# Optimization experiments

Hardware: AMD Instinct MI355X
Metric: run time of the kernel (lower is better)

The kernel has to match this reference:

```python
import jax, jax.numpy as jnp
import numpy as np

TAG = 64
START = 0
END = 1
NEG = -10000.0


def setup_inputs() -> dict:
    key = jax.random.key(0)
    kf, kw, kl = jax.random.split(key, 3)
    B, T, K = 1024, 512, TAG
    feats = jax.random.normal(kf, (B, T, K), dtype=jnp.float32)
    w = jax.random.uniform(kw, (K, K), minval=-1.0 / K, maxval=1.0 / K, dtype=jnp.float32)
    # default adjacency: forbid transitions into start (row START) and out of end (col END)
    adj = jnp.zeros((K, K), jnp.float32).at[START, :].set(1.0).at[:, END].set(1.0)
    weights = w + NEG * adj
    lens = jax.random.randint(kl, (B,), 1, T + 1)  # 1..T inclusive
    return {"feats": feats, "weights": weights, "lens": lens}


def reference(feats, weights, lens):
    # feats: [B, T, K], weights: [K, K] with weights[next, prev], lens: [B]
    B, T, K = feats.shape
    init = jnp.full((B, K), NEG, feats.dtype).at[:, START].set(0.0)
    mask_tb = (jnp.arange(T)[None, :] < lens[:, None]).T  # [T, B]
    ident = jnp.arange(K, dtype=jnp.int32)

    def step(fv, inp):
        feat, m = inp  # feat: [B, K], m: [B]
        scores = fv[:, None, :] + weights[None, :, :]  # [B, next, prev]
        new_fv = jnp.max(scores, axis=-1) + feat       # emission added after max
        bptr = jnp.argmax(scores, axis=-1).astype(jnp.int32)
        fv2 = jnp.where(m[:, None], new_fv, fv)
        bptr2 = jnp.where(m[:, None], bptr, ident[None, :])  # identity keeps backtrace valid past len
        return fv2, bptr2

    fv, bptrs = jax.lax.scan(step, init, (jnp.swapaxes(feats, 0, 1), mask_tb))
    terminal = fv + weights[END][None, :]              # transition to end tag
    best_last = jnp.argmax(terminal, axis=-1)
    path_score = jnp.take_along_axis(terminal, best_last[:, None], axis=1)[:, 0]

    def back(tag, bp):  # tag: [B], bp: [B, K]
        prev = jnp.take_along_axis(bp, tag[:, None], axis=1)[:, 0]
        return prev, tag  # emit tag chosen at this timestep

    _, path = jax.lax.scan(back, best_last.astype(jnp.int32), bptrs, reverse=True)
    best_paths = jnp.swapaxes(path, 0, 1)  # [B, T]; positions >= lens[b] are padding
    return path_score, best_paths
```

## Files before the change

### kernel.cpp

```cpp
#include <hip/hip_runtime.h>

#define TAGS 64
#define MAXT 512
#define NEG  -10000.0f
#define CH   8

__global__ __launch_bounds__(64, 1) void crf_viterbi(
    const float* __restrict__ feats,
    const float* __restrict__ weights,
    const int*   __restrict__ lens,
    float*       __restrict__ out,
    int B, int T)
{
    const int b    = blockIdx.x;
    const int lane = threadIdx.x;
    const int len  = lens[b];

    __shared__ float fv[TAGS];
    __shared__ float fbuf[2][CH * TAGS];
    __shared__ unsigned char  bptr[MAXT * TAGS];
    __shared__ unsigned short path[MAXT];

    float4 w4[16];
    #pragma unroll
    for (int i = 0; i < 16; ++i)
        w4[i] = *reinterpret_cast<const float4*>(weights + lane * TAGS + i * 4);
    const float wEnd = weights[1 * TAGS + lane];

    fv[lane] = (lane == 0) ? 0.0f : NEG;

    const float* fb  = feats + (size_t)b * T * TAGS;
    const int    lim = len * TAGS - 4;

    float nf = NEG;

#define F3(a, b, c) fmaxf(fmaxf((a), (b)), (c))
#define M3(a, b, c) min(min((a), (b)), (c))

    auto step = [&](int cbuf, int i, int t) {
        const float feat = fbuf[cbuf][i * TAGS + lane];
        float4 fq[16];
        #pragma unroll
        for (int g = 0; g < 16; ++g)
            fq[g] = *reinterpret_cast<const float4*>(&fv[g * 4]);
        float4 c4[16];
        #pragma unroll
        for (int g = 0; g < 16; ++g) {
            c4[g].x = fq[g].x + w4[g].x;
            c4[g].y = fq[g].y + w4[g].y;
            c4[g].z = fq[g].z + w4[g].z;
            c4[g].w = fq[g].w + w4[g].w;
        }
        const float* c = reinterpret_cast<const float*>(c4);

        float v1[22];
        #pragma unroll
        for (int k = 0; k < 21; ++k) v1[k] = F3(c[3*k], c[3*k+1], c[3*k+2]);
        v1[21] = c[63];
        float v2[8];
        #pragma unroll
        for (int k = 0; k < 7; ++k) v2[k] = F3(v1[3*k], v1[3*k+1], v1[3*k+2]);
        v2[7] = v1[21];
        const float v30 = F3(v2[0], v2[1], v2[2]);
        const float v31 = F3(v2[3], v2[4], v2[5]);
        const float v32 = fmaxf(v2[6], v2[7]);
        const float m   = F3(v30, v31, v32);

        nf = m + feat;
        fv[lane] = nf;

        unsigned e[64];
        #pragma unroll
        for (int p = 0; p < 64; ++p) {
            const float d = m - c[p];
            e[p] = (__float_as_uint(d) & 0xFFFFFFC0u) | (unsigned)p;
        }
        unsigned u1[22];
        #pragma unroll
        for (int k = 0; k < 21; ++k) u1[k] = M3(e[3*k], e[3*k+1], e[3*k+2]);
        u1[21] = e[63];
        unsigned u2[8];
        #pragma unroll
        for (int k = 0; k < 7; ++k) u2[k] = M3(u1[3*k], u1[3*k+1], u1[3*k+2]);
        u2[7] = u1[21];
        const unsigned u30 = M3(u2[0], u2[1], u2[2]);
        const unsigned u31 = M3(u2[3], u2[4], u2[5]);
        const unsigned u32 = min(u2[6], u2[7]);
        const unsigned idx = M3(u30, u31, u32);

        bptr[t * TAGS + lane] = (unsigned char)idx;
    };

    {
        int o0 = 4 * lane;        if (o0 > lim) o0 = lim;
        int o1 = 256 + 4 * lane;  if (o1 > lim) o1 = lim;
        *reinterpret_cast<float4*>(&fbuf[0][4 * lane])       = *reinterpret_cast<const float4*>(fb + o0);
        *reinterpret_cast<float4*>(&fbuf[0][256 + 4 * lane]) = *reinterpret_cast<const float4*>(fb + o1);
    }
    float4 n0, n1;
    {
        int o0 = CH * TAGS + 4 * lane;        if (o0 > lim) o0 = lim;
        int o1 = CH * TAGS + 256 + 4 * lane;  if (o1 > lim) o1 = lim;
        n0 = *reinterpret_cast<const float4*>(fb + o0);
        n1 = *reinterpret_cast<const float4*>(fb + o1);
    }

    int cb = 0;
    const int nfull = len / CH;
    for (int c = 0; c < nfull; ++c) {
        #pragma unroll
        for (int i = 0; i < CH; ++i) step(cb, i, c * CH + i);
        *reinterpret_cast<float4*>(&fbuf[cb ^ 1][4 * lane])       = n0;
        *reinterpret_cast<float4*>(&fbuf[cb ^ 1][256 + 4 * lane]) = n1;
        {
            int o0 = (c + 2) * CH * TAGS + 4 * lane;        if (o0 > lim) o0 = lim;
            int o1 = (c + 2) * CH * TAGS + 256 + 4 * lane;  if (o1 > lim) o1 = lim;
            n0 = *reinterpret_cast<const float4*>(fb + o0);
            n1 = *reinterpret_cast<const float4*>(fb + o1);
        }
        cb ^= 1;
    }
    const int rem = len - nfull * CH;
    for (int i = 0; i < rem; ++i) step(cb, i, nfull * CH + i);

    float tv = nf + wEnd;
    int   ti = lane;
    #pragma unroll
    for (int off = 32; off >= 1; off >>= 1) {
        const float ov = __shfl_xor(tv, off);
        const int   oi = __shfl_xor(ti, off);
        if (ov > tv || (ov == tv && oi < ti)) { tv = ov; ti = oi; }
    }
    if (lane == 0) out[b] = tv;
    const int bestlast = ti;

    for (int t = lane; t < T; t += 64)
        if (t >= len - 1) path[t] = (unsigned short)bestlast;
    __builtin_amdgcn_wave_barrier();

    if (lane == 0) {
        int tag = bestlast;
        for (int t = len - 1; t >= 1; --t) {
            tag = bptr[t * TAGS + tag];
            path[t - 1] = (unsigned short)tag;
        }
    }
    __builtin_amdgcn_wave_barrier();

    float* pout = out + B + (size_t)b * T;
    for (int t = lane; t < T; t += 64)
        pout[t] = (float)path[t];
}

extern "C" void kernel_launch(void* const* d_in, const int* in_sizes, int n_in,
                              void* d_out, int out_size, void* d_ws, size_t ws_size,
                              hipStream_t stream) {
    const float* feats   = (const float*)d_in[0];
    const float* weights = (const float*)d_in[1];
    const int*   lens    = (const int*)d_in[2];
    float*       out     = (float*)d_out;

    const int B = in_sizes[2];
    const int T = in_sizes[0] / (B * TAGS);

    crf_viterbi<<<dim3(B), dim3(64), 0, stream>>>(feats, weights, lens, out, B, T);
}
```

Baseline: 450.9 us.

## Split Viterbi max and argmax across waves with chunk-level software pipelining

The block grows from one wave to three. Wave 0 runs the serial max recurrence and publishes the forward values and maxima for each chunk into a triple-buffered shared array. Waves 1 and 2 compute the backpointer argmax for the previous chunk in parallel, alternating timesteps. This takes the argmax work off the serial critical path. The cost is a block-wide barrier per chunk, more shared memory, and three times the registers per block.

```diff
diff --git a/kernel.cpp b/kernel.cpp
--- a/kernel.cpp
+++ b/kernel.cpp
@@ -5,7 +5,7 @@
 #define NEG  -10000.0f
 #define CH   8
 
-__global__ __launch_bounds__(64, 1) void crf_viterbi(
+__global__ __launch_bounds__(192) void crf_viterbi(
     const float* __restrict__ feats,
     const float* __restrict__ weights,
     const int*   __restrict__ lens,
@@ -13,13 +13,18 @@
     int B, int T)
 {
     const int b    = blockIdx.x;
-    const int lane = threadIdx.x;
+    const int tid  = threadIdx.x;
+    const int wv   = tid >> 6;
+    const int lane = tid & 63;
     const int len  = lens[b];
 
-    __shared__ float fv[TAGS];
     __shared__ float fbuf[2][CH * TAGS];
+    __shared__ float pub[3][CH][2][TAGS];
     __shared__ unsigned char  bptr[MAXT * TAGS];
     __shared__ unsigned short path[MAXT];
+
+#define F3(a, b, c) fmaxf(fmaxf((a), (b)), (c))
+#define M3(a, b, c) min(min((a), (b)), (c))
 
     float4 w4[16];
     #pragma unroll
@@ -27,101 +32,119 @@
         w4[i] = *reinterpret_cast<const float4*>(weights + lane * TAGS + i * 4);
     const float wEnd = weights[1 * TAGS + lane];
 
-    fv[lane] = (lane == 0) ? 0.0f : NEG;
-
     const float* fb  = feats + (size_t)b * T * TAGS;
     const int    lim = len * TAGS - 4;
+    const int    nch = (len + CH - 1) / CH;
 
     float nf = NEG;
+    float4 n0 = {0,0,0,0}, n1 = {0,0,0,0};
+    int cb = 0;
 
-#define F3(a, b, c) fmaxf(fmaxf((a), (b)), (c))
-#define M3(a, b, c) min(min((a), (b)), (c))
-
-    auto step = [&](int cbuf, int i, int t) {
-        const float feat = fbuf[cbuf][i * TAGS + lane];
-        float4 fq[16];
-        #pragma unroll
-        for (int g = 0; g < 16; ++g)
-            fq[g] = *reinterpret_cast<const float4*>(&fv[g * 4]);
-        float4 c4[16];
-        #pragma unroll
-        for (int g = 0; g < 16; ++g) {
-            c4[g].x = fq[g].x + w4[g].x;
-            c4[g].y = fq[g].y + w4[g].y;
-            c4[g].z = fq[g].z + w4[g].z;
-            c4[g].w = fq[g].w + w4[g].w;
-        }
-        const float* c = reinterpret_cast<const float*>(c4);
-
-        float v1[22];
-        #pragma unroll
-        for (int k = 0; k < 21; ++k) v1[k] = F3(c[3*k], c[3*k+1], c[3*k+2]);
-        v1[21] = c[63];
-        float v2[8];
-        #pragma unroll
-        for (int k = 0; k < 7; ++k) v2[k] = F3(v1[3*k], v1[3*k+1], v1[3*k+2]);
-        v2[7] = v1[21];
-        const float v30 = F3(v2[0], v2[1], v2[2]);
-        const float v31 = F3(v2[3], v2[4], v2[5]);
-        const float v32 = fmaxf(v2[6], v2[7]);
-        const float m   = F3(v30, v31, v32);
-
-        nf = m + feat;
-        fv[lane] = nf;
-
-        unsigned e[64];
-        #pragma unroll
-        for (int p = 0; p < 64; ++p) {
-            const float d = m - c[p];
-            e[p] = (__float_as_uint(d) & 0xFFFFFFC0u) | (unsigned)p;
-        }
-        unsigned u1[22];
-        #pragma unroll
-        for (int k = 0; k < 21; ++k) u1[k] = M3(e[3*k], e[3*k+1], e[3*k+2]);
-        u1[21] = e[63];
-        unsigned u2[8];
-        #pragma unroll
-        for (int k = 0; k < 7; ++k) u2[k] = M3(u1[3*k], u1[3*k+1], u1[3*k+2]);
-        u2[7] = u1[21];
-        const unsigned u30 = M3(u2[0], u2[1], u2[2]);
-        const unsigned u31 = M3(u2[3], u2[4], u2[5]);
-        const unsigned u32 = min(u2[6], u2[7]);
-        const unsigned idx = M3(u30, u31, u32);
-
-        bptr[t * TAGS + lane] = (unsigned char)idx;
-    };
-
-    {
+    if (wv == 0) {
+        pub[2][CH - 1][0][lane] = (lane == 0) ? 0.0f : NEG;
         int o0 = 4 * lane;        if (o0 > lim) o0 = lim;
         int o1 = 256 + 4 * lane;  if (o1 > lim) o1 = lim;
         *reinterpret_cast<float4*>(&fbuf[0][4 * lane])       = *reinterpret_cast<const float4*>(fb + o0);
         *reinterpret_cast<float4*>(&fbuf[0][256 + 4 * lane]) = *reinterpret_cast<const float4*>(fb + o1);
+        int p0 = CH * TAGS + 4 * lane;        if (p0 > lim) p0 = lim;
+        int p1 = CH * TAGS + 256 + 4 * lane;  if (p1 > lim) p1 = lim;
+        n0 = *reinterpret_cast<const float4*>(fb + p0);
+        n1 = *reinterpret_cast<const float4*>(fb + p1);
     }
-    float4 n0, n1;
-    {
-        int o0 = CH * TAGS + 4 * lane;        if (o0 > lim) o0 = lim;
-        int o1 = CH * TAGS + 256 + 4 * lane;  if (o1 > lim) o1 = lim;
-        n0 = *reinterpret_cast<const float4*>(fb + o0);
-        n1 = *reinterpret_cast<const float4*>(fb + o1);
+    __syncthreads();
+
+    int m0 = 0;
+    for (int c = 0; c <= nch; ++c) {
+        const int m1 = (m0 == 0) ? 2 : m0 - 1;
+        const int m2 = (m0 == 2) ? 0 : m0 + 1;
+
+        if (wv == 0) {
+            if (c < nch) {
+                const int n = min(CH, len - c * CH);
+                float*       pw  = &pub[m0][0][0][0];
+                const float* pr0 = &pub[m1][CH - 1][0][0];
+                #pragma unroll
+                for (int i = 0; i < CH; ++i) {
+                    if (i < n) {
+                        const float feat = fbuf[cb][i * TAGS + lane];
+                        const float* fvp = (i == 0) ? pr0 : (pw + (i - 1) * 2 * TAGS);
+                        float4 fq[16];
+                        #pragma unroll
+                        for (int g = 0; g < 16; ++g)
+                            fq[g] = *reinterpret_cast<const float4*>(fvp + 4 * g);
+                        float4 c4[16];
+                        #pragma unroll
+                        for (int g = 0; g < 16; ++g) {
+                            c4[g].x = fq[g].x + w4[g].x;
+                            c4[g].y = fq[g].y + w4[g].y;
+                            c4[g].z = fq[g].z + w4[g].z;
+                            c4[g].w = fq[g].w + w4[g].w;
+                        }
+                        const float* cc = reinterpret_cast<const float*>(c4);
+                        float v1[22];
+                        #pragma unroll
+                        for (int k = 0; k < 21; ++k) v1[k] = F3(cc[3*k], cc[3*k+1], cc[3*k+2]);
+                        v1[21] = cc[63];
+                        float v2[8];
+                        #pragma unroll
+                        for (int k = 0; k < 7; ++k) v2[k] = F3(v1[3*k], v1[3*k+1], v1[3*k+2]);
+                        v2[7] = v1[21];
+                        const float v30 = F3(v2[0], v2[1], v2[2]);
+                        const float v31 = F3(v2[3], v2[4], v2[5]);
+                        const float v32 = fmaxf(v2[6], v2[7]);
+                        const float m   = F3(v30, v31, v32);
+
+                        nf = m + feat;
+                        pw[i * 2 * TAGS + lane]        = nf;
+                        pw[i * 2 * TAGS + TAGS + lane] = m;
+                    }
+                }
+                *reinterpret_cast<float4*>(&fbuf[cb ^ 1][4 * lane])       = n0;
+                *reinterpret_cast<float4*>(&fbuf[cb ^ 1][256 + 4 * lane]) = n1;
+                int q0 = (c + 2) * CH * TAGS + 4 * lane;        if (q0 > lim) q0 = lim;
+                int q1 = (c + 2) * CH * TAGS + 256 + 4 * lane;  if (q1 > lim) q1 = lim;
+                n0 = *reinterpret_cast<const float4*>(fb + q0);
+                n1 = *reinterpret_cast<const float4*>(fb + q1);
+                cb ^= 1;
+            }
+        } else if (c > 0) {
+            const int ck = c - 1;
+            const int n  = min(CH, len - ck * CH);
+            const float* prd = &pub[m1][0][0][0];
+            const float* pr0 = &pub[m2][CH - 1][0][0];
+            for (int i = wv - 1; i < n; i += 2) {
+                const float* fvp = (i == 0) ? pr0 : (prd + (i - 1) * 2 * TAGS);
+                const float  mm  = prd[i * 2 * TAGS + TAGS + lane];
+                unsigned q[16];
+                #pragma unroll
+                for (int g = 0; g < 16; ++g) {
+                    const float4 fq = *reinterpret_cast<const float4*>(fvp + 4 * g);
+                    const float cx = fq.x + w4[g].x;
+                    const float cy = fq.y + w4[g].y;
+                    const float cz = fq.z + w4[g].z;
+                    const float cw = fq.w + w4[g].w;
+                    const unsigned k0 = (__float_as_uint(mm - cx) & 0xFFFFFFC0u) | (unsigned)(4*g+0);
+                    const unsigned k1 = (__float_as_uint(mm - cy) & 0xFFFFFFC0u) | (unsigned)(4*g+1);
+                    const unsigned k2 = (__float_as_uint(mm - cz) & 0xFFFFFFC0u) | (unsigned)(4*g+2);
+                    const unsigned k3 = (__float_as_uint(mm - cw) & 0xFFFFFFC0u) | (unsigned)(4*g+3);
+                    q[g] = min(M3(k0, k1, k2), k3);
+                }
+                const unsigned t0 = M3(q[0],  q[1],  q[2]);
+                const unsigned t1 = M3(q[3],  q[4],  q[5]);
+                const unsigned t2 = M3(q[6],  q[7],  q[8]);
+                const unsigned t3 = M3(q[9],  q[10], q[11]);
+                const unsigned t4 = M3(q[12], q[13], q[14]);
+                const unsigned s0 = M3(t0, t1, t2);
+                const unsigned s1 = M3(t3, t4, q[15]);
+                const unsigned idx = min(s0, s1);
+                bptr[(ck * CH + i) * TAGS + lane] = (unsigned char)idx;
+            }
+        }
+        __syncthreads();
+        m0 = m2;
     }
 
-    int cb = 0;
-    const int nfull = len / CH;
-    for (int c = 0; c < nfull; ++c) {
-        #pragma unroll
-        for (int i = 0; i < CH; ++i) step(cb, i, c * CH + i);
-        *reinterpret_cast<float4*>(&fbuf[cb ^ 1][4 * lane])       = n0;
-        *reinterpret_cast<float4*>(&fbuf[cb ^ 1][256 + 4 * lane]) = n1;
-        {
-            int o0 = (c + 2) * CH * TAGS + 4 * lane;        if (o0 > lim) o0 = lim;
-            int o1 = (c + 2) * CH * TAGS + 256 + 4 * lane;  if (o1 > lim) o1 = lim;
-            n0 = *reinterpret_cast<const float4*>(fb + o0);
-            n1 = *reinterpret_cast<const float4*>(fb + o1);
-        }
-        cb ^= 1;
-    }
-    const int rem = len - nfull * CH;
-    for (int i = 0; i < rem; ++i) step(cb, i, nfull * CH + i);
+    if (wv != 0) return;
 
     float tv = nf + wEnd;
     int   ti = lane;
@@ -163,5 +186,5 @@
     const int B = in_sizes[2];
     const int T = in_sizes[0] / (B * TAGS);
 
-    crf_viterbi<<<dim3(B), dim3(64), 0, stream>>>(feats, weights, lens, out, B, T);
+    crf_viterbi<<<dim3(B), dim3(192), 0, stream>>>(feats, weights, lens, out, B, T);
 }
```

Result: slower. 500.4 us (+11.0%).

## Split forward pass across two redundant waves sharing argmax work, separate backtrace

Applied to the files above, without the earlier changes.

The forward max recurrence now runs in two blocks per sequence. Each computes the full max chain but performs the argmax only on alternate timesteps, writing backpointers to a global workspace. A second kernel copies those backpointers into LDS and does the serial backtrace. Feature prefetch moves from an LDS double buffer to registers. This halves argmax work on the critical path and frees LDS so more blocks fit per CU, at the cost of duplicated max work, global backpointer traffic and an extra launch. The old single kernel remains as a fallback when the workspace is too small.

```diff
diff --git a/kernel.cpp b/kernel.cpp
--- a/kernel.cpp
+++ b/kernel.cpp
@@ -5,21 +5,25 @@
 #define NEG  -10000.0f
 #define CH   8
 
-__global__ __launch_bounds__(64, 1) void crf_viterbi(
+
+#define F3(a, b, c) fmaxf(fmaxf((a), (b)), (c))
+#define M3(a, b, c) min(min((a), (b)), (c))
+
+__global__ __launch_bounds__(64, 1) void crf_forward(
     const float* __restrict__ feats,
     const float* __restrict__ weights,
     const int*   __restrict__ lens,
     float*       __restrict__ out,
+    unsigned char* __restrict__ gb,
+    int*         __restrict__ bestl,
     int B, int T)
 {
-    const int b    = blockIdx.x;
+    const int b    = blockIdx.x >> 1;
+    const int role = blockIdx.x & 1;
     const int lane = threadIdx.x;
     const int len  = lens[b];
 
     __shared__ float fv[TAGS];
-    __shared__ float fbuf[2][CH * TAGS];
-    __shared__ unsigned char  bptr[MAXT * TAGS];
-    __shared__ unsigned short path[MAXT];
 
     float4 w4[16];
     #pragma unroll
@@ -30,15 +34,24 @@
     fv[lane] = (lane == 0) ? 0.0f : NEG;
 
     const float* fb  = feats + (size_t)b * T * TAGS;
-    const int    lim = len * TAGS - 4;
+    const int    cap = len * TAGS;
+    unsigned char* gbb = gb + (size_t)b * T * TAGS + lane;
 
     float nf = NEG;
 
-#define F3(a, b, c) fmaxf(fmaxf((a), (b)), (c))
-#define M3(a, b, c) min(min((a), (b)), (c))
-
-    auto step = [&](int cbuf, int i, int t) {
-        const float feat = fbuf[cbuf][i * TAGS + lane];
+    float fcur[CH], fnx[CH];
+    #pragma unroll
+    for (int i = 0; i < CH; ++i) {
+        int o = i * TAGS + lane; if (o >= cap) o = lane;
+        fcur[i] = fb[o];
+    }
+    #pragma unroll
+    for (int i = 0; i < CH; ++i) {
+        int o = (CH + i) * TAGS + lane; if (o >= cap) o = lane;
+        fnx[i] = fb[o];
+    }
+
+    auto step = [&](float feat, int t, bool doArg) {
         float4 fq[16];
         #pragma unroll
         for (int g = 0; g < 16; ++g)
@@ -69,12 +82,151 @@
         nf = m + feat;
         fv[lane] = nf;
 
+        if (doArg) {
+            unsigned q[16];
+            #pragma unroll
+            for (int g = 0; g < 16; ++g) {
+                const unsigned k0 = (__float_as_uint(m - c[4*g+0]) & 0xFFFFFFC0u) | (unsigned)(4*g+0);
+                const unsigned k1 = (__float_as_uint(m - c[4*g+1]) & 0xFFFFFFC0u) | (unsigned)(4*g+1);
+                const unsigned k2 = (__float_as_uint(m - c[4*g+2]) & 0xFFFFFFC0u) | (unsigned)(4*g+2);
+                const unsigned k3 = (__float_as_uint(m - c[4*g+3]) & 0xFFFFFFC0u) | (unsigned)(4*g+3);
+                q[g] = min(M3(k0, k1, k2), k3);
+            }
+            const unsigned t0 = M3(q[0],  q[1],  q[2]);
+            const unsigned t1 = M3(q[3],  q[4],  q[5]);
+            const unsigned t2 = M3(q[6],  q[7],  q[8]);
+            const unsigned t3 = M3(q[9],  q[10], q[11]);
+            const unsigned t4 = M3(q[12], q[13], q[14]);
+            const unsigned idx = min(M3(t0, t1, t2), M3(t3, t4, q[15]));
+            gbb[(size_t)t * TAGS] = (unsigned char)idx;
+        }
+    };
+
+    const int nfull = len / CH;
+    for (int c = 0; c < nfull; ++c) {
+        #pragma unroll
+        for (int i = 0; i < CH; ++i)
+            step(fcur[i], c * CH + i, (i & 1) == role);
+        #pragma unroll
+        for (int i = 0; i < CH; ++i) fcur[i] = fnx[i];
+        #pragma unroll
+        for (int i = 0; i < CH; ++i) {
+            int o = (c + 2) * CH * TAGS + i * TAGS + lane;
+            if (o >= cap) o = lane;
+            fnx[i] = fb[o];
+        }
+    }
+    const int rem = len - nfull * CH;
+    #pragma unroll
+    for (int i = 0; i < CH; ++i)
+        if (i < rem) step(fcur[i], nfull * CH + i, (i & 1) == role);
+
+    if (role != 0) return;
+
+    float tv = nf + wEnd;
+    int   ti = lane;
+    #pragma unroll
+    for (int off = 32; off >= 1; off >>= 1) {
+        const float ov = __shfl_xor(tv, off);
+        const int   oi = __shfl_xor(ti, off);
+        if (ov > tv || (ov == tv && oi < ti)) { tv = ov; ti = oi; }
+    }
+    if (lane == 0) { out[b] = tv; bestl[b] = ti; }
+}
+
+__global__ __launch_bounds__(64, 1) void crf_backtrace(
+    const int*           __restrict__ lens,
+    const unsigned char* __restrict__ gb,
+    const int*           __restrict__ bestl,
+    float*               __restrict__ out,
+    int B, int T)
+{
+    const int b    = blockIdx.x;
+    const int lane = threadIdx.x;
+    const int len  = lens[b];
+
+    __shared__ unsigned char  bptr[MAXT * TAGS];
+    __shared__ unsigned short path[MAXT];
+
+    const uint4* src = reinterpret_cast<const uint4*>(gb + (size_t)b * T * TAGS);
+    uint4*       dst = reinterpret_cast<uint4*>(bptr);
+    const int n16 = len * (TAGS / 16);
+    for (int i = lane; i < n16; i += 64) dst[i] = src[i];
+
+    const int bestlast = bestl[b];
+    for (int t = lane; t < T; t += 64)
+        if (t >= len - 1) path[t] = (unsigned short)bestlast;
+    __syncthreads();
+
+    if (lane == 0) {
+        int tag = bestlast;
+        for (int t = len - 1; t >= 1; --t) {
+            tag = bptr[t * TAGS + tag];
+            path[t - 1] = (unsigned short)tag;
+        }
+    }
+    __syncthreads();
+
+    float* pout = out + B + (size_t)b * T;
+    for (int t = lane; t < T; t += 64)
+        pout[t] = (float)path[t];
+}
+
+__global__ __launch_bounds__(64, 1) void crf_viterbi(
+    const float* __restrict__ feats, const float* __restrict__ weights,
+    const int* __restrict__ lens, float* __restrict__ out, int B, int T)
+{
+    const int b    = blockIdx.x;
+    const int lane = threadIdx.x;
+    const int len  = lens[b];
+
+    __shared__ float fv[TAGS];
+    __shared__ float fbuf[2][CH * TAGS];
+    __shared__ unsigned char  bptr[MAXT * TAGS];
+    __shared__ unsigned short path[MAXT];
+
+    float4 w4[16];
+    #pragma unroll
+    for (int i = 0; i < 16; ++i)
+        w4[i] = *reinterpret_cast<const float4*>(weights + lane * TAGS + i * 4);
+    const float wEnd = weights[1 * TAGS + lane];
+
+    fv[lane] = (lane == 0) ? 0.0f : NEG;
+    const float* fb  = feats + (size_t)b * T * TAGS;
+    const int    lim = len * TAGS - 4;
+    float nf = NEG;
+
+    auto step = [&](int cbuf, int i, int t) {
+        const float feat = fbuf[cbuf][i * TAGS + lane];
+        float4 fq[16];
+        #pragma unroll
+        for (int g = 0; g < 16; ++g)
+            fq[g] = *reinterpret_cast<const float4*>(&fv[g * 4]);
+        float4 c4[16];
+        #pragma unroll
+        for (int g = 0; g < 16; ++g) {
+            c4[g].x = fq[g].x + w4[g].x;
+            c4[g].y = fq[g].y + w4[g].y;
+            c4[g].z = fq[g].z + w4[g].z;
+            c4[g].w = fq[g].w + w4[g].w;
+        }
+        const float* c = reinterpret_cast<const float*>(c4);
+        float v1[22];
+        #pragma unroll
+        for (int k = 0; k < 21; ++k) v1[k] = F3(c[3*k], c[3*k+1], c[3*k+2]);
+        v1[21] = c[63];
+        float v2[8];
+        #pragma unroll
+        for (int k = 0; k < 7; ++k) v2[k] = F3(v1[3*k], v1[3*k+1], v1[3*k+2]);
+        v2[7] = v1[21];
+        const float m = F3(F3(v2[0], v2[1], v2[2]),
+                           F3(v2[3], v2[4], v2[5]), fmaxf(v2[6], v2[7]));
+        nf = m + feat;
+        fv[lane] = nf;
         unsigned e[64];
         #pragma unroll
-        for (int p = 0; p < 64; ++p) {
-            const float d = m - c[p];
-            e[p] = (__float_as_uint(d) & 0xFFFFFFC0u) | (unsigned)p;
-        }
+        for (int p = 0; p < 64; ++p)
+            e[p] = (__float_as_uint(m - c[p]) & 0xFFFFFFC0u) | (unsigned)p;
         unsigned u1[22];
         #pragma unroll
         for (int k = 0; k < 21; ++k) u1[k] = M3(e[3*k], e[3*k+1], e[3*k+2]);
@@ -83,11 +235,8 @@
         #pragma unroll
         for (int k = 0; k < 7; ++k) u2[k] = M3(u1[3*k], u1[3*k+1], u1[3*k+2]);
         u2[7] = u1[21];
-        const unsigned u30 = M3(u2[0], u2[1], u2[2]);
-        const unsigned u31 = M3(u2[3], u2[4], u2[5]);
-        const unsigned u32 = min(u2[6], u2[7]);
-        const unsigned idx = M3(u30, u31, u32);
-
+        const unsigned idx = M3(M3(u2[0], u2[1], u2[2]),
+                                M3(u2[3], u2[4], u2[5]), min(u2[6], u2[7]));
         bptr[t * TAGS + lane] = (unsigned char)idx;
     };
 
@@ -104,7 +253,6 @@
         n0 = *reinterpret_cast<const float4*>(fb + o0);
         n1 = *reinterpret_cast<const float4*>(fb + o1);
     }
-
     int cb = 0;
     const int nfull = len / CH;
     for (int c = 0; c < nfull; ++c) {
@@ -133,11 +281,9 @@
     }
     if (lane == 0) out[b] = tv;
     const int bestlast = ti;
-
     for (int t = lane; t < T; t += 64)
         if (t >= len - 1) path[t] = (unsigned short)bestlast;
     __builtin_amdgcn_wave_barrier();
-
     if (lane == 0) {
         int tag = bestlast;
         for (int t = len - 1; t >= 1; --t) {
@@ -146,7 +292,6 @@
         }
     }
     __builtin_amdgcn_wave_barrier();
-
     float* pout = out + B + (size_t)b * T;
     for (int t = lane; t < T; t += 64)
         pout[t] = (float)path[t];
@@ -163,5 +308,13 @@
     const int B = in_sizes[2];
     const int T = in_sizes[0] / (B * TAGS);
 
-    crf_viterbi<<<dim3(B), dim3(64), 0, stream>>>(feats, weights, lens, out, B, T);
+    const size_t need = (size_t)B * T * TAGS + (size_t)B * sizeof(int);
+    if (d_ws != nullptr && ws_size >= need) {
+        unsigned char* gb    = (unsigned char*)d_ws;
+        int*           bestl = (int*)((unsigned char*)d_ws + (size_t)B * T * TAGS);
+        crf_forward<<<dim3(2 * B), dim3(64), 0, stream>>>(feats, weights, lens, out, gb, bestl, B, T);
+        crf_backtrace<<<dim3(B), dim3(64), 0, stream>>>(lens, gb, bestl, out, B, T);
+    } else {
+        crf_viterbi<<<dim3(B), dim3(64), 0, stream>>>(feats, weights, lens, out, B, T);
+    }
 }
```

Result: slower. 472.1 us (+4.7%).
